# Kernel optimization log

Measured on AMD Instinct MI355X. Metric: run time of the kernel, lower is better.

## Reference

```python
import jax, jax.numpy as jnp
import numpy as np

B, S, E = 2, 4096, 512

def setup_inputs() -> dict:
    key = jax.random.key(0)
    kx, kq, kk, kv, ko = jax.random.split(key, 5)
    scale = 1.0 / np.sqrt(E)  # init-style scaling for weights
    return {
        "x": jax.random.normal(kx, (B, S, E), dtype=jnp.float32),
        "Wq": jax.random.normal(kq, (E, E), dtype=jnp.float32) * scale,
        "Wk": jax.random.normal(kk, (E, E), dtype=jnp.float32) * scale,
        "Wv": jax.random.normal(kv, (E, E), dtype=jnp.float32) * scale,
        "Wo": jax.random.normal(ko, (E, E), dtype=jnp.float32) * scale,
        "bo": jnp.zeros((E,), dtype=jnp.float32),
    }

def reference(x, Wq, Wk, Wv, Wo, bo):
    # nn.Linear: y = x @ W.T  (weights stored [out, in])
    q = jnp.einsum("bse,fe->bsf", x, Wq)
    k = jnp.einsum("bse,fe->bsf", x, Wk)
    v = jnp.einsum("bse,fe->bsf", x, Wv)
    inv_scale = 1.0 / jnp.sqrt(jnp.asarray(x.shape[-1], x.dtype))
    scores = jnp.einsum("bqe,bke->bqk", q, k) * inv_scale  # [B,S,S]
    S_len = x.shape[1]
    # torch.triu(ones) keeps j >= i; masked_fill where triu==0 masks j < i
    row = jnp.arange(S_len)[:, None]
    col = jnp.arange(S_len)[None, :]
    keep = col >= row  # [S,S], faithfully anti-causal as in the source
    scores = jnp.where(keep[None, :, :], scores, jnp.asarray(-jnp.inf, scores.dtype))
    attn = jax.nn.softmax(scores, axis=-1)
    # dropout p=0.0 -> identity
    out = jnp.einsum("bqk,bke->bqe", attn, v)
    return jnp.einsum("bse,fe->bsf", out, Wo) + bo
```

## Files before the change

### kernel.cpp

```cpp
#include <hip/hip_runtime.h>
#include <hip/hip_bf16.h>

#define S_LEN 4096
#define E_DIM 512
#define B_DIM 2
#define M_ROWS (B_DIM * S_LEN)

typedef __attribute__((ext_vector_type(8))) short short8;
typedef __attribute__((ext_vector_type(4))) float floatx4;

__device__ __forceinline__ unsigned short f2bf(float f) {
    unsigned u = __float_as_uint(f);
    unsigned r = (u + 0x7fffu + ((u >> 16) & 1u)) >> 16;
    return (unsigned short)r;
}
__device__ __forceinline__ float bf2f(unsigned short u) {
    return __uint_as_float((unsigned)u << 16);
}

__device__ __forceinline__ void async_copy16(unsigned short* lds, const unsigned short* g) {
    auto gp = (const __attribute__((address_space(1))) unsigned int*)g;
    auto lp = (__attribute__((address_space(3))) unsigned int*)lds;
    __builtin_amdgcn_global_load_lds(gp, lp, 16, 0, 0);
}

struct MapArg { unsigned short m[320]; };

__global__ __launch_bounds__(256) void convert_bf16(
    const float* __restrict__ x,  const float* __restrict__ wq,
    const float* __restrict__ wk, const float* __restrict__ wv,
    const float* __restrict__ wo, unsigned short* __restrict__ dst)
{
    long i = (long)blockIdx.x * 1024 + (long)threadIdx.x * 4;
    const float* src; long off;
    if      (i < 4194304) { src = x;  off = i; }
    else if (i < 4456448) { src = wq; off = i - 4194304; }
    else if (i < 4718592) { src = wk; off = i - 4456448; }
    else if (i < 4980736) { src = wv; off = i - 4718592; }
    else                  { src = wo; off = i - 4980736; }
    float4 v = *(const float4*)(src + off);
    ushort4 o;
    o.x = f2bf(v.x); o.y = f2bf(v.y); o.z = f2bf(v.z); o.w = f2bf(v.w);
    *(ushort4*)(dst + i) = o;
}

__device__ __forceinline__ void gemm_core(
    const unsigned short* __restrict__ A, const unsigned short* __restrict__ W,
    void* __restrict__ Cv, const float* __restrict__ bias, int mode,
    int m0, int n0)
{
    __shared__ unsigned short As[128 * 32];
    __shared__ unsigned short Bs[128 * 32];
    const int tid = threadIdx.x;
    const int lane = tid & 63, wave = tid >> 6;
    const int wm = wave >> 1, wn = wave & 1;
    const int q4 = lane >> 4, l16 = lane & 15;

    floatx4 acc[4][4];
#pragma unroll
    for (int i = 0; i < 4; ++i)
#pragma unroll
        for (int j = 0; j < 4; ++j) acc[i][j] = (floatx4){0.f, 0.f, 0.f, 0.f};

    const int srow = lane >> 2;
    const int scol = (lane & 3) * 8;

    for (int k0 = 0; k0 < 512; k0 += 32) {
        async_copy16(&As[(wave * 16) * 32],
                     A + (size_t)(m0 + wave * 16 + srow) * 512 + k0 + scol);
        async_copy16(&As[(64 + wave * 16) * 32],
                     A + (size_t)(m0 + 64 + wave * 16 + srow) * 512 + k0 + scol);
        async_copy16(&Bs[(wave * 16) * 32],
                     W + (size_t)(n0 + wave * 16 + srow) * 512 + k0 + scol);
        async_copy16(&Bs[(64 + wave * 16) * 32],
                     W + (size_t)(n0 + 64 + wave * 16 + srow) * 512 + k0 + scol);
        __syncthreads();
        short8 af[4], bfr[4];
#pragma unroll
        for (int i = 0; i < 4; ++i) {
            af[i]  = *(const short8*)&As[(wm * 64 + i * 16 + l16) * 32 + q4 * 8];
            bfr[i] = *(const short8*)&Bs[(wn * 64 + i * 16 + l16) * 32 + q4 * 8];
        }
#pragma unroll
        for (int i = 0; i < 4; ++i)
#pragma unroll
            for (int j = 0; j < 4; ++j)
                acc[i][j] = __builtin_amdgcn_mfma_f32_16x16x32_bf16(af[i], bfr[j], acc[i][j], 0, 0, 0);
        __syncthreads();
    }

    if (mode == 0) {
        unsigned short* C = (unsigned short*)Cv;
#pragma unroll
        for (int i = 0; i < 4; ++i) {
            int rowb = m0 + wm * 64 + i * 16 + q4 * 4;
#pragma unroll
            for (int j = 0; j < 4; ++j) {
                int col = n0 + wn * 64 + j * 16 + l16;
#pragma unroll
                for (int rg = 0; rg < 4; ++rg)
                    C[(size_t)(rowb + rg) * 512 + col] = f2bf(acc[i][j][rg]);
            }
        }
    } else if (mode == 1) {
        unsigned short* C = (unsigned short*)Cv;
#pragma unroll
        for (int i = 0; i < 4; ++i) {
            int grow = m0 + wm * 64 + i * 16 + q4 * 4;
            int b = grow >> 12, s = grow & 4095;
#pragma unroll
            for (int j = 0; j < 4; ++j) {
                int e = n0 + wn * 64 + j * 16 + l16;
                ushort4 pk;
                pk.x = f2bf(acc[i][j][0]); pk.y = f2bf(acc[i][j][1]);
                pk.z = f2bf(acc[i][j][2]); pk.w = f2bf(acc[i][j][3]);
                *(ushort4*)(C + (size_t)b * 512 * 4096 + (size_t)e * 4096 + s) = pk;
            }
        }
    } else {
        float* C = (float*)Cv;
#pragma unroll
        for (int i = 0; i < 4; ++i) {
            int rowb = m0 + wm * 64 + i * 16 + q4 * 4;
#pragma unroll
            for (int j = 0; j < 4; ++j) {
                int col = n0 + wn * 64 + j * 16 + l16;
                float bv = bias[col];
#pragma unroll
                for (int rg = 0; rg < 4; ++rg)
                    C[(size_t)(rowb + rg) * 512 + col] = acc[i][j][rg] + bv;
            }
        }
    }
}

__global__ __launch_bounds__(256) void gemm_qkv(
    const unsigned short* __restrict__ xb,
    const unsigned short* __restrict__ Wqb, const unsigned short* __restrict__ Wkb,
    const unsigned short* __restrict__ Wvb,
    unsigned short* __restrict__ Qb, unsigned short* __restrict__ Kb,
    unsigned short* __restrict__ Vtb)
{
    const int z = blockIdx.z;
    const unsigned short* W = (z == 0) ? Wqb : (z == 1) ? Wkb : Wvb;
    unsigned short* C = (z == 0) ? Qb : (z == 1) ? Kb : Vtb;
    gemm_core(xb, W, C, nullptr, (z == 2) ? 1 : 0, blockIdx.y * 128, blockIdx.x * 128);
}

__global__ __launch_bounds__(256) void gemm_out(
    const unsigned short* __restrict__ AOb, const unsigned short* __restrict__ Wob,
    const float* __restrict__ bo, float* __restrict__ out)
{
    gemm_core(AOb, Wob, out, bo, 2, blockIdx.y * 128, blockIdx.x * 128);
}

__global__ __launch_bounds__(512, 2) void flash_mfma(
    const unsigned short* __restrict__ Qg, const unsigned short* __restrict__ Kg,
    const unsigned short* __restrict__ Vt,
    unsigned short* __restrict__ Oh, float* __restrict__ Lb, MapArg map)
{
    const int enc = map.m[blockIdx.x];
    const int tile = enc & 63, ch = (enc >> 6) & 3, bb = enc >> 8;
    const int i0 = tile * 64;
    const int lo0 = 1024 * ch, hi = 1024 * ch + 1024;
    const int lo = (i0 > lo0) ? i0 : lo0;

    const int tid = threadIdx.x;
    const int lane = tid & 63, w = tid >> 6;
    const int s = w & 3, h = w >> 2;
    const int q4 = lane >> 4, l16 = lane & 15;
    const float scale = 0.044194173824159216f;
    const float MREF = 4.0f;

    __shared__ float Sred[4][64][36];
    __shared__ unsigned short Plds[64][40];
    __shared__ float Lred[64][8];

    const size_t rowbase = (size_t)bb * S_LEN;
    const size_t vbase   = (size_t)bb * 512 * 4096;

    short8 aq[4][4];
#pragma unroll
    for (int mg = 0; mg < 4; ++mg)
#pragma unroll
        for (int ks = 0; ks < 4; ++ks)
            aq[mg][ks] = *(const short8*)(Qg + (rowbase + i0 + mg * 16 + l16) * 512
                                          + s * 128 + ks * 32 + q4 * 8);

    floatx4 oacc[4][4];
#pragma unroll
    for (int mg = 0; mg < 4; ++mg)
#pragma unroll
        for (int nc = 0; nc < 4; ++nc) oacc[mg][nc] = (floatx4){0.f, 0.f, 0.f, 0.f};

    const int r = tid >> 3;
    const int g = tid & 7;
    float l_acc = 0.f;

    auto step = [&](int j0, short8 (&bkc)[4], short8 (&bkn)[4], int jn) {
        short8 vf[4];
#pragma unroll
        for (int nc = 0; nc < 4; ++nc)
            vf[nc] = *(const short8*)(Vt + vbase
                + (size_t)(w * 64 + nc * 16 + l16) * 4096 + j0 + q4 * 8);
#pragma unroll
        for (int ks = 0; ks < 4; ++ks)
            bkn[ks] = *(const short8*)(Kg + (rowbase + jn + h * 16 + l16) * 512
                                       + s * 128 + ks * 32 + q4 * 8);
        floatx4 sf[4];
#pragma unroll
        for (int mg = 0; mg < 4; ++mg) sf[mg] = (floatx4){0.f, 0.f, 0.f, 0.f};
#pragma unroll
        for (int ks = 0; ks < 4; ++ks)
#pragma unroll
            for (int mg = 0; mg < 4; ++mg)
                sf[mg] = __builtin_amdgcn_mfma_f32_16x16x32_bf16(
                    bkc[ks], aq[mg][ks], sf[mg], 0, 0, 0);
#pragma unroll
        for (int mg = 0; mg < 4; ++mg)
            *(floatx4*)&Sred[s][mg * 16 + l16][h * 16 + q4 * 4] = sf[mg];
        __syncthreads();

        float4 a0 = *(const float4*)&Sred[0][r][4 * g];
        float4 a1 = *(const float4*)&Sred[1][r][4 * g];
        float4 a2 = *(const float4*)&Sred[2][r][4 * g];
        float4 a3 = *(const float4*)&Sred[3][r][4 * g];
        float sv[4] = { a0.x + a1.x + a2.x + a3.x, a0.y + a1.y + a2.y + a3.y,
                        a0.z + a1.z + a2.z + a3.z, a0.w + a1.w + a2.w + a3.w };
        ushort4 pk;
        float p0, p1, p2, p3;
        {
            int key = j0 + 4 * g;
            int row = i0 + r;
            p0 = (key + 0 >= row) ? __expf(sv[0] * scale - MREF) : 0.f;
            p1 = (key + 1 >= row) ? __expf(sv[1] * scale - MREF) : 0.f;
            p2 = (key + 2 >= row) ? __expf(sv[2] * scale - MREF) : 0.f;
            p3 = (key + 3 >= row) ? __expf(sv[3] * scale - MREF) : 0.f;
        }
        l_acc += p0 + p1 + p2 + p3;
        pk.x = f2bf(p0); pk.y = f2bf(p1); pk.z = f2bf(p2); pk.w = f2bf(p3);
        *(ushort4*)&Plds[r][4 * g] = pk;
        __syncthreads();

        short8 ap[4];
#pragma unroll
        for (int mg = 0; mg < 4; ++mg)
            ap[mg] = *(const short8*)&Plds[mg * 16 + l16][q4 * 8];
#pragma unroll
        for (int mg = 0; mg < 4; ++mg)
#pragma unroll
            for (int nc = 0; nc < 4; ++nc)
                oacc[mg][nc] = __builtin_amdgcn_mfma_f32_16x16x32_bf16(
                    ap[mg], vf[nc], oacc[mg][nc], 0, 0, 0);
    };

    short8 bkA[4], bkB[4];
    int j0 = hi - 32;
#pragma unroll
    for (int ks = 0; ks < 4; ++ks)
        bkA[ks] = *(const short8*)(Kg + (rowbase + j0 + h * 16 + l16) * 512
                                   + s * 128 + ks * 32 + q4 * 8);
    while (j0 >= lo) {
        int jn = (j0 - 32 >= lo) ? j0 - 32 : lo;
        step(j0, bkA, bkB, jn);
        j0 -= 32;
        if (j0 < lo) break;
        jn = (j0 - 32 >= lo) ? j0 - 32 : lo;
        step(j0, bkB, bkA, jn);
        j0 -= 32;
    }
    __syncthreads();

    const int baseArr = (ch == 0) ? 0 : (ch == 1) ? 32 : (ch == 2) ? 96 : 192;
    const int slot = baseArr + bb * 16 * (ch + 1) + tile;

    Lred[r][g] = l_acc;
    __syncthreads();
    if (tid < 64) {
        float sum = 0.f;
#pragma unroll
        for (int gg = 0; gg < 8; ++gg) sum += Lred[tid][gg];
        Lb[(size_t)slot * 64 + tid] = sum;
    }

    unsigned short* Op = Oh + (size_t)slot * 64 * 512;
#pragma unroll
    for (int mg = 0; mg < 4; ++mg)
#pragma unroll
        for (int nc = 0; nc < 4; ++nc)
#pragma unroll
            for (int rg = 0; rg < 4; ++rg)
                Op[(size_t)(mg * 16 + q4 * 4 + rg) * 512 + w * 64 + nc * 16 + l16]
                    = f2bf(oacc[mg][nc][rg]);
}

__global__ __launch_bounds__(256) void flash_merge(
    const unsigned short* __restrict__ Oh, const float* __restrict__ Lb,
    unsigned short* __restrict__ AO)
{
    const int row = blockIdx.x;
    const int c = threadIdx.x * 2;
    const int bb = row >> 12, i = row & 4095;
    const int t = i >> 6, ri = i & 63;
    const int chmin = i >> 10;
    float lsum = 0.f, v0 = 0.f, v1 = 0.f;
#pragma unroll
    for (int ch = 0; ch < 4; ++ch) {
        if (ch < chmin) continue;
        int baseArr = (ch == 0) ? 0 : (ch == 1) ? 32 : (ch == 2) ? 96 : 192;
        int slot = baseArr + bb * 16 * (ch + 1) + t;
        lsum += Lb[(size_t)slot * 64 + ri];
        const unsigned short* p = Oh + (size_t)slot * 64 * 512 + (size_t)ri * 512 + c;
        v0 += bf2f(p[0]);
        v1 += bf2f(p[1]);
    }
    float inv = 1.f / lsum;
    ushort2 o; o.x = f2bf(v0 * inv); o.y = f2bf(v1 * inv);
    *(ushort2*)(AO + (size_t)row * 512 + c) = o;
}

static MapArg build_map() {
    int enc[320], steps[320], n = 0;
    for (int bb = 0; bb < 2; ++bb)
        for (int ch = 0; ch < 4; ++ch)
            for (int t = 0; t < 16 * (ch + 1) && t < 64; ++t) {
                int i0 = t * 64, lo0 = 1024 * ch, hi = lo0 + 1024;
                int lo = (i0 > lo0) ? i0 : lo0;
                enc[n] = t | (ch << 6) | (bb << 8);
                steps[n] = (hi - lo) / 32;
                ++n;
            }
    for (int i = 1; i < n; ++i) {
        int e = enc[i], st = steps[i], j = i - 1;
        while (j >= 0 && steps[j] > st) {
            steps[j + 1] = steps[j]; enc[j + 1] = enc[j]; --j;
        }
        steps[j + 1] = st; enc[j + 1] = e;
    }
    MapArg mp{};
    for (int c = 0; c < 64; ++c) {
        mp.m[c]       = (unsigned short)enc[127 - c];
        mp.m[256 + c] = (unsigned short)enc[c];
    }
    for (int k = 0; k < 192; ++k)
        mp.m[64 + k] = (unsigned short)enc[128 + k];
    return mp;
}

extern "C" void kernel_launch(void* const* d_in, const int* in_sizes, int n_in,
                              void* d_out, int out_size, void* d_ws, size_t ws_size,
                              hipStream_t stream) {
    (void)in_sizes; (void)n_in; (void)out_size; (void)ws_size;
    const float* x  = (const float*)d_in[0];
    const float* Wq = (const float*)d_in[1];
    const float* Wk = (const float*)d_in[2];
    const float* Wv = (const float*)d_in[3];
    const float* Wo = (const float*)d_in[4];
    const float* bo = (const float*)d_in[5];
    float* out = (float*)d_out;

    unsigned short* xb  = (unsigned short*)d_ws;
    unsigned short* Wqb = xb  + 4194304;
    unsigned short* Wkb = Wqb + 262144;
    unsigned short* Wvb = Wkb + 262144;
    unsigned short* Wob = Wvb + 262144;
    unsigned short* Qb  = Wob + 262144;
    unsigned short* Kb  = Qb  + 4194304;
    unsigned short* Vtb = Kb  + 4194304;
    unsigned short* AOb = Vtb + 4194304;
    unsigned short* Ohb = AOb + 4194304;
    float* Lbf = (float*)(Ohb + 10485760);

    static const MapArg mp = build_map();

    convert_bf16<<<5120, 256, 0, stream>>>(x, Wq, Wk, Wv, Wo, xb);

    gemm_qkv<<<dim3(4, 64, 3), 256, 0, stream>>>(xb, Wqb, Wkb, Wvb, Qb, Kb, Vtb);

    flash_mfma<<<320, 512, 0, stream>>>(Qb, Kb, Vtb, Ohb, Lbf, mp);

    flash_merge<<<8192, 256, 0, stream>>>(Ohb, Lbf, AOb);

    gemm_out<<<dim3(4, 64), 256, 0, stream>>>(AOb, Wob, bo, out);
}
```

Before: 231.8 us.

## Split attention keys into eight chunks, rebalance block map, raise MFMA wave priority

The flash kernel now splits the key range into eight 512-wide chunks instead of four 1024-wide chunks, giving 576 blocks instead of 320. The schedule map is rebuilt as a bucketed assignment that pairs long and short blocks across three dispatch waves. MFMA sections are wrapped in s_setprio, and the workspace is reorganised so the partial outputs alias the no-longer-needed bf16 inputs and AO reuses the Q buffer. The aim is better CU load balance and a smaller memory footprint, at the cost of more partial outputs for the merge kernel to read and sum.

```diff
diff --git a/kernel.cpp b/kernel.cpp
--- a/kernel.cpp
+++ b/kernel.cpp
@@ -24,24 +24,25 @@
     __builtin_amdgcn_global_load_lds(gp, lp, 16, 0, 0);
 }
 
-struct MapArg { unsigned short m[320]; };
+struct MapArg { unsigned short m[576]; };
 
 __global__ __launch_bounds__(256) void convert_bf16(
     const float* __restrict__ x,  const float* __restrict__ wq,
     const float* __restrict__ wk, const float* __restrict__ wv,
-    const float* __restrict__ wo, unsigned short* __restrict__ dst)
+    const float* __restrict__ wo, unsigned short* __restrict__ dstU,
+    unsigned short* __restrict__ dstWo)
 {
     long i = (long)blockIdx.x * 1024 + (long)threadIdx.x * 4;
-    const float* src; long off;
-    if      (i < 4194304) { src = x;  off = i; }
-    else if (i < 4456448) { src = wq; off = i - 4194304; }
-    else if (i < 4718592) { src = wk; off = i - 4456448; }
-    else if (i < 4980736) { src = wv; off = i - 4718592; }
-    else                  { src = wo; off = i - 4980736; }
+    const float* src; long off; unsigned short* dst; long doff;
+    if      (i < 4194304) { src = x;  off = i;           dst = dstU;  doff = i; }
+    else if (i < 4456448) { src = wq; off = i - 4194304; dst = dstU;  doff = i; }
+    else if (i < 4718592) { src = wk; off = i - 4456448; dst = dstU;  doff = i; }
+    else if (i < 4980736) { src = wv; off = i - 4718592; dst = dstU;  doff = i; }
+    else                  { src = wo; off = i - 4980736; dst = dstWo; doff = i - 4980736; }
     float4 v = *(const float4*)(src + off);
     ushort4 o;
     o.x = f2bf(v.x); o.y = f2bf(v.y); o.z = f2bf(v.z); o.w = f2bf(v.w);
-    *(ushort4*)(dst + i) = o;
+    *(ushort4*)(dst + doff) = o;
 }
 
 __device__ __forceinline__ void gemm_core(
@@ -160,9 +161,9 @@
     unsigned short* __restrict__ Oh, float* __restrict__ Lb, MapArg map)
 {
     const int enc = map.m[blockIdx.x];
-    const int tile = enc & 63, ch = (enc >> 6) & 3, bb = enc >> 8;
+    const int tile = enc & 63, ch = (enc >> 6) & 7, bb = enc >> 9;
     const int i0 = tile * 64;
-    const int lo0 = 1024 * ch, hi = 1024 * ch + 1024;
+    const int lo0 = 512 * ch, hi = lo0 + 512;
     const int lo = (i0 > lo0) ? i0 : lo0;
 
     const int tid = threadIdx.x;
@@ -210,12 +211,14 @@
         floatx4 sf[4];
 #pragma unroll
         for (int mg = 0; mg < 4; ++mg) sf[mg] = (floatx4){0.f, 0.f, 0.f, 0.f};
+        __builtin_amdgcn_s_setprio(1);
 #pragma unroll
         for (int ks = 0; ks < 4; ++ks)
 #pragma unroll
             for (int mg = 0; mg < 4; ++mg)
                 sf[mg] = __builtin_amdgcn_mfma_f32_16x16x32_bf16(
                     bkc[ks], aq[mg][ks], sf[mg], 0, 0, 0);
+        __builtin_amdgcn_s_setprio(0);
 #pragma unroll
         for (int mg = 0; mg < 4; ++mg)
             *(floatx4*)&Sred[s][mg * 16 + l16][h * 16 + q4 * 4] = sf[mg];
@@ -246,12 +249,14 @@
 #pragma unroll
         for (int mg = 0; mg < 4; ++mg)
             ap[mg] = *(const short8*)&Plds[mg * 16 + l16][q4 * 8];
+        __builtin_amdgcn_s_setprio(1);
 #pragma unroll
         for (int mg = 0; mg < 4; ++mg)
 #pragma unroll
             for (int nc = 0; nc < 4; ++nc)
                 oacc[mg][nc] = __builtin_amdgcn_mfma_f32_16x16x32_bf16(
                     ap[mg], vf[nc], oacc[mg][nc], 0, 0, 0);
+        __builtin_amdgcn_s_setprio(0);
     };
 
     short8 bkA[4], bkB[4];
@@ -271,8 +276,7 @@
     }
     __syncthreads();
 
-    const int baseArr = (ch == 0) ? 0 : (ch == 1) ? 32 : (ch == 2) ? 96 : 192;
-    const int slot = baseArr + bb * 16 * (ch + 1) + tile;
+    const int slot = 8 * ch * (ch + 1) + bb * 8 * (ch + 1) + tile;
 
     Lred[r][g] = l_acc;
     __syncthreads();
@@ -302,13 +306,10 @@
     const int c = threadIdx.x * 2;
     const int bb = row >> 12, i = row & 4095;
     const int t = i >> 6, ri = i & 63;
-    const int chmin = i >> 10;
+    const int chmin = i >> 9;
     float lsum = 0.f, v0 = 0.f, v1 = 0.f;
-#pragma unroll
-    for (int ch = 0; ch < 4; ++ch) {
-        if (ch < chmin) continue;
-        int baseArr = (ch == 0) ? 0 : (ch == 1) ? 32 : (ch == 2) ? 96 : 192;
-        int slot = baseArr + bb * 16 * (ch + 1) + t;
+    for (int ch = chmin; ch < 8; ++ch) {
+        int slot = 8 * ch * (ch + 1) + bb * 8 * (ch + 1) + t;
         lsum += Lb[(size_t)slot * 64 + ri];
         const unsigned short* p = Oh + (size_t)slot * 64 * 512 + (size_t)ri * 512 + c;
         v0 += bf2f(p[0]);
@@ -320,30 +321,45 @@
 }
 
 static MapArg build_map() {
-    int enc[320], steps[320], n = 0;
+    int enc[576], steps[576], n = 0;
     for (int bb = 0; bb < 2; ++bb)
-        for (int ch = 0; ch < 4; ++ch)
-            for (int t = 0; t < 16 * (ch + 1) && t < 64; ++t) {
-                int i0 = t * 64, lo0 = 1024 * ch, hi = lo0 + 1024;
+        for (int ch = 0; ch < 8; ++ch)
+            for (int t = 0; t < 8 * (ch + 1); ++t) {
+                int i0 = t * 64, lo0 = 512 * ch, hi = lo0 + 512;
                 int lo = (i0 > lo0) ? i0 : lo0;
-                enc[n] = t | (ch << 6) | (bb << 8);
+                enc[n] = t | (ch << 6) | (bb << 9);
                 steps[n] = (hi - lo) / 32;
                 ++n;
             }
-    for (int i = 1; i < n; ++i) {
-        int e = enc[i], st = steps[i], j = i - 1;
-        while (j >= 0 && steps[j] > st) {
-            steps[j + 1] = steps[j]; enc[j + 1] = enc[j]; --j;
-        }
-        steps[j + 1] = st; enc[j + 1] = e;
-    }
+    static int buck[9][576];
+    int bn[9] = {0};
+    for (int i = 0; i < n; ++i) { int b = steps[i] >> 1; buck[b][bn[b]++] = enc[i]; }
     MapArg mp{};
-    for (int c = 0; c < 64; ++c) {
-        mp.m[c]       = (unsigned short)enc[127 - c];
-        mp.m[256 + c] = (unsigned short)enc[c];
-    }
-    for (int k = 0; k < 192; ++k)
-        mp.m[64 + k] = (unsigned short)enc[128 + k];
+    int a = 0;
+    for (int c = 0; c < 16; ++c) {
+        mp.m[c] = (unsigned short)buck[8][a++];
+        mp.m[256 + c] = (unsigned short)buck[8][a++];
+        mp.m[512 + c] = (unsigned short)buck[1][c];
+    }
+    for (int c = 16; c < 32; ++c) {
+        mp.m[c] = (unsigned short)buck[8][a++];
+        mp.m[256 + c] = (unsigned short)buck[7][c - 16];
+        mp.m[512 + c] = (unsigned short)buck[2][c - 16];
+    }
+    for (int c = 32; c < 48; ++c) {
+        mp.m[c] = (unsigned short)buck[8][a++];
+        mp.m[256 + c] = (unsigned short)buck[6][c - 32];
+        mp.m[512 + c] = (unsigned short)buck[3][c - 32];
+    }
+    for (int c = 48; c < 64; ++c) {
+        mp.m[c] = (unsigned short)buck[8][a++];
+        mp.m[256 + c] = (unsigned short)buck[5][c - 48];
+        mp.m[512 + c] = (unsigned short)buck[4][c - 48];
+    }
+    for (int c = 64; c < 256; ++c) {
+        mp.m[c] = (unsigned short)buck[8][a++];
+        mp.m[256 + c] = (unsigned short)buck[8][a++];
+    }
     return mp;
 }
 
@@ -359,27 +375,28 @@
     const float* bo = (const float*)d_in[5];
     float* out = (float*)d_out;
 
-    unsigned short* xb  = (unsigned short*)d_ws;
-    unsigned short* Wqb = xb  + 4194304;
+    unsigned short* ws  = (unsigned short*)d_ws;
+    unsigned short* Wob = ws;
+    unsigned short* QAb = ws + 262144;
+    unsigned short* Kb  = QAb + 4194304;
+    unsigned short* Vtb = Kb + 4194304;
+    unsigned short* U   = Vtb + 4194304;
+    unsigned short* xb  = U;
+    unsigned short* Wqb = U + 4194304;
     unsigned short* Wkb = Wqb + 262144;
     unsigned short* Wvb = Wkb + 262144;
-    unsigned short* Wob = Wvb + 262144;
-    unsigned short* Qb  = Wob + 262144;
-    unsigned short* Kb  = Qb  + 4194304;
-    unsigned short* Vtb = Kb  + 4194304;
-    unsigned short* AOb = Vtb + 4194304;
-    unsigned short* Ohb = AOb + 4194304;
-    float* Lbf = (float*)(Ohb + 10485760);
+    unsigned short* Ohb = U;
+    float* Lbf = (float*)(U + 18874368);
 
     static const MapArg mp = build_map();
 
-    convert_bf16<<<5120, 256, 0, stream>>>(x, Wq, Wk, Wv, Wo, xb);
-
-    gemm_qkv<<<dim3(4, 64, 3), 256, 0, stream>>>(xb, Wqb, Wkb, Wvb, Qb, Kb, Vtb);
-
-    flash_mfma<<<320, 512, 0, stream>>>(Qb, Kb, Vtb, Ohb, Lbf, mp);
-
-    flash_merge<<<8192, 256, 0, stream>>>(Ohb, Lbf, AOb);
-
-    gemm_out<<<dim3(4, 64), 256, 0, stream>>>(AOb, Wob, bo, out);
-}
+    convert_bf16<<<5120, 256, 0, stream>>>(x, Wq, Wk, Wv, Wo, U, Wob);
+
+    gemm_qkv<<<dim3(4, 64, 3), 256, 0, stream>>>(xb, Wqb, Wkb, Wvb, QAb, Kb, Vtb);
+
+    flash_mfma<<<576, 512, 0, stream>>>(QAb, Kb, Vtb, Ohb, Lbf, mp);
+
+    flash_merge<<<8192, 256, 0, stream>>>(Ohb, Lbf, QAb);
+
+    gemm_out<<<dim3(4, 64), 256, 0, stream>>>(QAb, Wob, bo, out);
+}
```

New measurement: 233.0 us. About the same (+0.6%).
